# Kernel optimization log

Measured on AMD Instinct MI355X. Metric: run time of the kernel, lower is better.

The kernel has to match this reference:

```python
import jax, jax.numpy as jnp
import numpy as np

# module-level constants from the original repo
NUM_CLASSES = 4
CLASS_NONE = 0
RETINA_SIZE = 224.0

# loss weights (ContourLoss defaults)
POINT_W, ORIENT_W, CLASS_W, INTERSECT_W = 1.0, 0.5, 1.0, 0.1

B, S = 8, 2048


def setup_inputs() -> dict:
    key = jax.random.key(0)
    k1, k2, k3, k4, k5, k6, k7 = jax.random.split(key, 7)
    point_pred = jax.random.uniform(k1, (B, S, 2), jnp.float32) * RETINA_SIZE
    orient_pred = jax.random.normal(k2, (B, S, 2), jnp.float32)
    orient_pred = orient_pred / jnp.linalg.norm(orient_pred, axis=-1, keepdims=True)
    class_pred = jax.random.normal(k3, (B, S, NUM_CLASSES), jnp.float32)
    tgt_pts = jax.random.uniform(k4, (B, S, 2), jnp.float32) * RETINA_SIZE
    tgt_orient = jax.random.normal(k5, (B, S, 2), jnp.float32)
    tgt_orient = tgt_orient / jnp.linalg.norm(tgt_orient, axis=-1, keepdims=True)
    tgt_cls = jax.random.randint(k6, (B, S), 0, NUM_CLASSES).astype(jnp.float32)
    target_seq = jnp.concatenate([tgt_pts, tgt_orient, tgt_cls[..., None]], axis=-1)
    padding_mask = jax.random.bernoulli(k7, 0.15, (B, S))
    return {"point_pred": point_pred, "orient_pred": orient_pred,
            "class_pred": class_pred, "target_seq": target_seq,
            "padding_mask": padding_mask}


def _intersection_per_sample(pts, non_none):
    # pts: (S,2), non_none: (S,) bool.
    # Compact valid points to the front (stable), mirroring point_pred[b, valid_idx].
    order = jnp.argsort(jnp.logical_not(non_none), stable=True)
    pts_c = pts[order]                      # (S,2), first n rows valid
    n = non_none.sum()
    n_seg = n - 1
    starts, ends = pts_c[:-1], pts_c[1:]    # (S-1,2)
    M = S - 1
    ii = jnp.arange(M)[:, None]
    jj = jnp.arange(M)[None, :]
    mask = ((jj >= ii + 2) & (ii < n_seg) & (jj < n_seg)
            & ~((ii == 0) & (jj == n_seg - 1)) & (n >= 4))
    p1 = starts[:, None, :]; p2 = ends[:, None, :]   # segment i
    p3 = starts[None, :, :]; p4 = ends[None, :, :]   # segment j

    def cross(a, b, c):
        return ((b[..., 0] - a[..., 0]) * (c[..., 1] - a[..., 1])
                - (b[..., 1] - a[..., 1]) * (c[..., 0] - a[..., 0]))

    d1 = cross(p3, p4, p1)
    d2 = cross(p3, p4, p2)
    d3 = cross(p1, p2, p3)
    d4 = cross(p1, p2, p4)
    s = jax.nn.sigmoid(-d1 * d2 * 0.01) * jax.nn.sigmoid(-d3 * d4 * 0.01)
    return jnp.where(mask, s, 0.0).sum(), mask.sum()


def reference(point_pred, orient_pred, class_pred, target_seq, padding_mask):
    Bd, Sd, _ = class_pred.shape
    target_class = target_seq[:, :, 4].astype(jnp.int32)
    target_point = target_seq[:, :, :2]
    target_orient = target_seq[:, :, 2:4]
    valid = jnp.logical_not(padding_mask)
    valid_f = valid.astype(jnp.float32)

    # classification: cross entropy, masked mean over valid tokens
    logp = jax.nn.log_softmax(class_pred, axis=-1)
    cls = -jnp.take_along_axis(logp, target_class[..., None], axis=-1)[..., 0]
    cls_loss = (cls * valid_f).sum() / jnp.maximum(valid_f.sum(), 1.0)

    non_none = valid & (target_class != CLASS_NONE)
    nn_f = non_none.astype(jnp.float32)
    nn_denom = jnp.maximum(nn_f.sum(), 1.0)

    # point: SmoothL1 (beta=1) on normalized coords, mean over xy, masked mean
    d = (point_pred - target_point) / RETINA_SIZE
    ad = jnp.abs(d)
    sl1 = jnp.where(ad < 1.0, 0.5 * d * d, ad - 0.5).mean(axis=-1)
    pt_loss = (sl1 * nn_f).sum() / nn_denom

    # orientation: 1 - cosine similarity (orient_pred assumed L2-normalized)
    cos_sim = (orient_pred * target_orient).sum(axis=-1)
    orient_loss = ((1.0 - cos_sim) * nn_f).sum() / nn_denom

    # intersection penalty over non-adjacent segment pairs, per sample
    sums, counts = jax.vmap(_intersection_per_sample)(point_pred, non_none)
    cnt = counts.sum()
    intersect_loss = jnp.where(cnt > 0, sums.sum() / jnp.maximum(cnt, 1).astype(jnp.float32), 0.0)

    total = (POINT_W * pt_loss + ORIENT_W * orient_loss
             + CLASS_W * cls_loss + INTERSECT_W * intersect_loss)
    return (total, pt_loss, orient_loss, cls_loss, intersect_loss)
```

## Files before the change

kernel.cpp:

```cpp
#include <hip/hip_runtime.h>

#define B 8
#define S 2048
#define NBPS 64
#define NBLK (B * NBPS)
#define TPB 256
#define LPB (S / NBPS)


__global__ __launch_bounds__(TPB) void mega_kernel(
    const float2* __restrict__ point_pred,
    const float2* __restrict__ orient_pred,
    const float4* __restrict__ class_pred,
    const float*  __restrict__ target_seq,
    const int*    __restrict__ padding_mask,
    int*   __restrict__ n_buf,
    float* __restrict__ partial,
    float* __restrict__ acc2)
{
    __shared__ float2 sp[S];
    __shared__ float red[TPB / 64][1];
    __shared__ int wsum[TPB / 64], woff[TPB / 64], nTot;

    const int blk = blockIdx.x;
    const int tid = threadIdx.x;
    const int lane = tid & 63, wv = tid >> 6;
    const int b = blk >> 6;
    const int iblk = blk & (NBPS - 1);
    const int base = b * S;
    const int e0 = tid * 8;

    const int4* pm4 = (const int4*)(padding_mask + base + e0);
    const int4 ma = pm4[0], mb = pm4[1];
    const float4* tr4 = (const float4*)(target_seq + (size_t)(base + e0) * 5);
    float4 tq[10];
    #pragma unroll
    for (int k = 0; k < 10; ++k) tq[k] = tr4[k];
    float t4v[8];
    t4v[0] = tq[1].x; t4v[1] = tq[2].y; t4v[2] = tq[3].z; t4v[3] = tq[4].w;
    t4v[4] = tq[6].x; t4v[5] = tq[7].y; t4v[6] = tq[8].z; t4v[7] = tq[9].w;
    const float4* pq4 = (const float4*)(point_pred + base + e0);
    const float4 pa = pq4[0], pb = pq4[1], pc = pq4[2], pd = pq4[3];
    float2 p[8];
    p[0] = make_float2(pa.x, pa.y); p[1] = make_float2(pa.z, pa.w);
    p[2] = make_float2(pb.x, pb.y); p[3] = make_float2(pb.z, pb.w);
    p[4] = make_float2(pc.x, pc.y); p[5] = make_float2(pc.z, pc.w);
    p[6] = make_float2(pd.x, pd.y); p[7] = make_float2(pd.z, pd.w);
    int f[8];
    f[0] = (ma.x == 0 && (int)t4v[0] != 0) ? 1 : 0;
    f[1] = (ma.y == 0 && (int)t4v[1] != 0) ? 1 : 0;
    f[2] = (ma.z == 0 && (int)t4v[2] != 0) ? 1 : 0;
    f[3] = (ma.w == 0 && (int)t4v[3] != 0) ? 1 : 0;
    f[4] = (mb.x == 0 && (int)t4v[4] != 0) ? 1 : 0;
    f[5] = (mb.y == 0 && (int)t4v[5] != 0) ? 1 : 0;
    f[6] = (mb.z == 0 && (int)t4v[6] != 0) ? 1 : 0;
    f[7] = (mb.w == 0 && (int)t4v[7] != 0) ? 1 : 0;

    float cls_a = 0.f, pt_a = 0.f, or_a = 0.f, v_a = 0.f, nn_a = 0.f;
    if (tid < LPB) {
        const int idx = base + iblk * LPB + tid;
        const bool valid = (padding_mask[idx] == 0);
        const float* row = target_seq + (size_t)idx * 5;
        const float t4 = row[4];
        const int tc = (int)t4;
        const bool nn = valid && (tc != 0);
        if (valid) {
            const float4 cl = class_pred[idx];
            const float m = fmaxf(fmaxf(cl.x, cl.y), fmaxf(cl.z, cl.w));
            const float lse = m + logf(expf(cl.x - m) + expf(cl.y - m) +
                                       expf(cl.z - m) + expf(cl.w - m));
            const float ct = (tc == 0) ? cl.x : (tc == 1) ? cl.y : (tc == 2) ? cl.z : cl.w;
            cls_a = lse - ct;
            v_a = 1.f;
        }
        if (nn) {
            const float2 pp = point_pred[idx];
            const float dx = (pp.x - row[0]) * (1.0f / 224.0f);
            const float dy = (pp.y - row[1]) * (1.0f / 224.0f);
            const float adx = fabsf(dx), ady = fabsf(dy);
            const float l0 = (adx < 1.f) ? 0.5f * dx * dx : adx - 0.5f;
            const float l1 = (ady < 1.f) ? 0.5f * dy * dy : ady - 0.5f;
            pt_a = 0.5f * (l0 + l1);
            const float2 op = orient_pred[idx];
            or_a = 1.f - (op.x * row[2] + op.y * row[3]);
            nn_a = 1.f;
        }
    }
    if (wv == 0) {
        #pragma unroll
        for (int off = 32; off > 0; off >>= 1) {
            cls_a += __shfl_down(cls_a, (unsigned)off, 64);
            pt_a  += __shfl_down(pt_a,  (unsigned)off, 64);
            or_a  += __shfl_down(or_a,  (unsigned)off, 64);
            v_a   += __shfl_down(v_a,   (unsigned)off, 64);
            nn_a  += __shfl_down(nn_a,  (unsigned)off, 64);
        }
        if (lane == 0) {
            acc2[0 * NBLK + blk] = cls_a;
            acc2[1 * NBLK + blk] = pt_a;
            acc2[2 * NBLK + blk] = or_a;
            acc2[3 * NBLK + blk] = v_a;
            acc2[4 * NBLK + blk] = nn_a;
        }
    }

    const int c = f[0]+f[1]+f[2]+f[3]+f[4]+f[5]+f[6]+f[7];
    int inc = c;
    #pragma unroll
    for (int off = 1; off < 64; off <<= 1) {
        int u = __shfl_up(inc, (unsigned)off, 64);
        if (lane >= off) inc += u;
    }
    if (lane == 63) wsum[wv] = inc;
    __syncthreads();
    if (tid == 0) {
        int run = 0;
        #pragma unroll
        for (int w = 0; w < TPB / 64; ++w) { woff[w] = run; run += wsum[w]; }
        nTot = run;
    }
    __syncthreads();
    int pos = woff[wv] + inc - c;
    #pragma unroll
    for (int k = 0; k < 8; ++k) { if (f[k]) sp[pos++] = p[k]; }
    __syncthreads();

    const int n = nTot;
    if (iblk == 0 && tid == 0) n_buf[b] = n;

    float local = 0.f;
    if (n >= 4) {
        const int n_seg = n - 1;
        for (int i = iblk; i < n_seg - 2; i += NBPS) {
            const float2 q1 = sp[i], q2 = sp[i + 1];
            const float e12x = q2.x - q1.x, e12y = q2.y - q1.y;
            const int jmax = (i == 0) ? n_seg - 1 : n_seg;
            for (int j = i + 2 + tid; j < jmax; j += TPB) {
                const float2 q3 = sp[j], q4 = sp[j + 1];
                const float e34x = q4.x - q3.x, e34y = q4.y - q3.y;
                const float ce = e12x * e34y - e12y * e34x;
                const float rx = q1.x - q3.x, ry = q1.y - q3.y;
                const float d1 = e34x * ry - e34y * rx;
                const float d3 = e12y * rx - e12x * ry;
                const float d2 = d1 - ce;
                const float d4 = d3 + ce;
                const float ea = __expf(d1 * d2 * 0.01f);
                const float eb = __expf(d3 * d4 * 0.01f);
                local += __builtin_amdgcn_rcpf((1.f + ea) * (1.f + eb));
            }
        }
    }
    #pragma unroll
    for (int off = 32; off > 0; off >>= 1)
        local += __shfl_down(local, (unsigned)off, 64);
    if (lane == 0) red[wv][0] = local;
    __syncthreads();
    if (tid == 0)
        partial[blk] = red[0][0] + red[1][0] + red[2][0] + red[3][0];
}

__global__ __launch_bounds__(64) void finalize_kernel(
    const float* __restrict__ acc2,
    const int* __restrict__ n_buf,
    const float* __restrict__ partial,
    float* __restrict__ out)
{
    const int lane = threadIdx.x;

    const float4* p4 = (const float4*)partial;
    const float4 u = p4[lane * 2], v = p4[lane * 2 + 1];
    float s = (u.x + u.y) + (u.z + u.w) + (v.x + v.y) + (v.z + v.w);

    float a[5];
    #pragma unroll
    for (int ch = 0; ch < 5; ++ch) {
        const float4* c4 = (const float4*)(acc2 + ch * NBLK);
        const float4 x = c4[lane * 2], y = c4[lane * 2 + 1];
        a[ch] = (x.x + x.y) + (x.z + x.w) + (y.x + y.y) + (y.z + y.w);
    }

    #pragma unroll
    for (int off = 32; off > 0; off >>= 1) {
        s += __shfl_down(s, (unsigned)off, 64);
        #pragma unroll
        for (int ch = 0; ch < 5; ++ch)
            a[ch] += __shfl_down(a[ch], (unsigned)off, 64);
    }

    if (lane == 0) {
        const float inter_sum = s;
        long long cnt = 0;
        #pragma unroll
        for (int b2 = 0; b2 < B; ++b2) {
            const int n = n_buf[b2];
            if (n >= 4) {
                const long long ns = n - 1;
                cnt += (ns - 1) * (ns - 2) / 2 - 1;
            }
        }
        const float cls_loss = a[0] / fmaxf(a[3], 1.f);
        const float pt_loss = a[1] / fmaxf(a[4], 1.f);
        const float orient_loss = a[2] / fmaxf(a[4], 1.f);
        const float intersect_loss = (cnt > 0) ? inter_sum / (float)cnt : 0.f;
        out[0] = 1.0f * pt_loss + 0.5f * orient_loss +
                 1.0f * cls_loss + 0.1f * intersect_loss;
        out[1] = pt_loss;
        out[2] = orient_loss;
        out[3] = cls_loss;
        out[4] = intersect_loss;
    }
}

extern "C" void kernel_launch(void* const* d_in, const int* in_sizes, int n_in,
                              void* d_out, int out_size, void* d_ws, size_t ws_size,
                              hipStream_t stream) {
    (void)in_sizes; (void)n_in; (void)out_size; (void)ws_size;
    const float2* point_pred  = (const float2*)d_in[0];
    const float2* orient_pred = (const float2*)d_in[1];
    const float4* class_pred  = (const float4*)d_in[2];
    const float*  target_seq  = (const float*)d_in[3];
    const int*    padding_mask = (const int*)d_in[4];

    int*   n_buf   = (int*)d_ws;
    float* partial = (float*)((char*)d_ws + 64);
    float* acc2    = (float*)((char*)d_ws + 2176);

    mega_kernel<<<NBLK, TPB, 0, stream>>>(point_pred, orient_pred, class_pred,
                                          target_seq, padding_mask,
                                          n_buf, partial, acc2);
    finalize_kernel<<<1, 64, 0, stream>>>(acc2, n_buf, partial, (float*)d_out);
}
```

Baseline: 22.20 us.

## Split loss and intersection work into separate blocks and double intersection blocks per sample

Intersection blocks per sample go from 64 to 128, so each block handles fewer segment rows i, giving 1024 intersection blocks. The per-element loss terms move out of those blocks into 64 dedicated blocks that use all 256 threads, and each block reduces the five accumulators in shared memory before writing them. The finalize kernel is updated for the new partial and accumulator layouts. In exchange, every intersection block still reloads and compacts its whole sample, so that redundant load and scan work now happens twice as often.

```diff
diff --git a/kernel.cpp b/kernel.cpp
--- a/kernel.cpp
+++ b/kernel.cpp
@@ -2,10 +2,11 @@
 
 #define B 8
 #define S 2048
-#define NBPS 64
-#define NBLK (B * NBPS)
+#define NBPS 128
+#define NBLK_INTER (B * NBPS)
+#define NBLK_LOSS 64
+#define NBLK_TOTAL (NBLK_INTER + NBLK_LOSS)
 #define TPB 256
-#define LPB (S / NBPS)
 
 
 __global__ __launch_bounds__(TPB) void mega_kernel(
@@ -19,51 +20,105 @@
     float* __restrict__ acc2)
 {
     __shared__ float2 sp[S];
-    __shared__ float red[TPB / 64][1];
+    __shared__ float red[TPB / 64][5];
     __shared__ int wsum[TPB / 64], woff[TPB / 64], nTot;
 
     const int blk = blockIdx.x;
     const int tid = threadIdx.x;
     const int lane = tid & 63, wv = tid >> 6;
-    const int b = blk >> 6;
-    const int iblk = blk & (NBPS - 1);
-    const int base = b * S;
-    const int e0 = tid * 8;
-
-    const int4* pm4 = (const int4*)(padding_mask + base + e0);
-    const int4 ma = pm4[0], mb = pm4[1];
-    const float4* tr4 = (const float4*)(target_seq + (size_t)(base + e0) * 5);
-    float4 tq[10];
-    #pragma unroll
-    for (int k = 0; k < 10; ++k) tq[k] = tr4[k];
-    float t4v[8];
-    t4v[0] = tq[1].x; t4v[1] = tq[2].y; t4v[2] = tq[3].z; t4v[3] = tq[4].w;
-    t4v[4] = tq[6].x; t4v[5] = tq[7].y; t4v[6] = tq[8].z; t4v[7] = tq[9].w;
-    const float4* pq4 = (const float4*)(point_pred + base + e0);
-    const float4 pa = pq4[0], pb = pq4[1], pc = pq4[2], pd = pq4[3];
-    float2 p[8];
-    p[0] = make_float2(pa.x, pa.y); p[1] = make_float2(pa.z, pa.w);
-    p[2] = make_float2(pb.x, pb.y); p[3] = make_float2(pb.z, pb.w);
-    p[4] = make_float2(pc.x, pc.y); p[5] = make_float2(pc.z, pc.w);
-    p[6] = make_float2(pd.x, pd.y); p[7] = make_float2(pd.z, pd.w);
-    int f[8];
-    f[0] = (ma.x == 0 && (int)t4v[0] != 0) ? 1 : 0;
-    f[1] = (ma.y == 0 && (int)t4v[1] != 0) ? 1 : 0;
-    f[2] = (ma.z == 0 && (int)t4v[2] != 0) ? 1 : 0;
-    f[3] = (ma.w == 0 && (int)t4v[3] != 0) ? 1 : 0;
-    f[4] = (mb.x == 0 && (int)t4v[4] != 0) ? 1 : 0;
-    f[5] = (mb.y == 0 && (int)t4v[5] != 0) ? 1 : 0;
-    f[6] = (mb.z == 0 && (int)t4v[6] != 0) ? 1 : 0;
-    f[7] = (mb.w == 0 && (int)t4v[7] != 0) ? 1 : 0;
-
-    float cls_a = 0.f, pt_a = 0.f, or_a = 0.f, v_a = 0.f, nn_a = 0.f;
-    if (tid < LPB) {
-        const int idx = base + iblk * LPB + tid;
+
+    if (blk < NBLK_INTER) {
+        const int b = blk >> 7;
+        const int iblk = blk & (NBPS - 1);
+        const int base = b * S;
+        const int e0 = tid * 8;
+
+        const int4* pm4 = (const int4*)(padding_mask + base + e0);
+        const int4 ma = pm4[0], mb = pm4[1];
+        const float4* tr4 = (const float4*)(target_seq + (size_t)(base + e0) * 5);
+        float4 tq[10];
+        #pragma unroll
+        for (int k = 0; k < 10; ++k) tq[k] = tr4[k];
+        float t4v[8];
+        t4v[0] = tq[1].x; t4v[1] = tq[2].y; t4v[2] = tq[3].z; t4v[3] = tq[4].w;
+        t4v[4] = tq[6].x; t4v[5] = tq[7].y; t4v[6] = tq[8].z; t4v[7] = tq[9].w;
+        const float4* pq4 = (const float4*)(point_pred + base + e0);
+        const float4 pa = pq4[0], pb = pq4[1], pc = pq4[2], pd = pq4[3];
+        float2 p[8];
+        p[0] = make_float2(pa.x, pa.y); p[1] = make_float2(pa.z, pa.w);
+        p[2] = make_float2(pb.x, pb.y); p[3] = make_float2(pb.z, pb.w);
+        p[4] = make_float2(pc.x, pc.y); p[5] = make_float2(pc.z, pc.w);
+        p[6] = make_float2(pd.x, pd.y); p[7] = make_float2(pd.z, pd.w);
+        int f[8];
+        f[0] = (ma.x == 0 && (int)t4v[0] != 0) ? 1 : 0;
+        f[1] = (ma.y == 0 && (int)t4v[1] != 0) ? 1 : 0;
+        f[2] = (ma.z == 0 && (int)t4v[2] != 0) ? 1 : 0;
+        f[3] = (ma.w == 0 && (int)t4v[3] != 0) ? 1 : 0;
+        f[4] = (mb.x == 0 && (int)t4v[4] != 0) ? 1 : 0;
+        f[5] = (mb.y == 0 && (int)t4v[5] != 0) ? 1 : 0;
+        f[6] = (mb.z == 0 && (int)t4v[6] != 0) ? 1 : 0;
+        f[7] = (mb.w == 0 && (int)t4v[7] != 0) ? 1 : 0;
+
+        const int c = f[0]+f[1]+f[2]+f[3]+f[4]+f[5]+f[6]+f[7];
+        int inc = c;
+        #pragma unroll
+        for (int off = 1; off < 64; off <<= 1) {
+            int u = __shfl_up(inc, (unsigned)off, 64);
+            if (lane >= off) inc += u;
+        }
+        if (lane == 63) wsum[wv] = inc;
+        __syncthreads();
+        if (tid == 0) {
+            int run = 0;
+            #pragma unroll
+            for (int w = 0; w < TPB / 64; ++w) { woff[w] = run; run += wsum[w]; }
+            nTot = run;
+        }
+        __syncthreads();
+        int pos = woff[wv] + inc - c;
+        #pragma unroll
+        for (int k = 0; k < 8; ++k) { if (f[k]) sp[pos++] = p[k]; }
+        __syncthreads();
+
+        const int n = nTot;
+        if (iblk == 0 && tid == 0) n_buf[b] = n;
+
+        float local = 0.f;
+        if (n >= 4) {
+            const int n_seg = n - 1;
+            for (int i = iblk; i < n_seg - 2; i += NBPS) {
+                const float2 q1 = sp[i], q2 = sp[i + 1];
+                const float e12x = q2.x - q1.x, e12y = q2.y - q1.y;
+                const int jmax = (i == 0) ? n_seg - 1 : n_seg;
+                for (int j = i + 2 + tid; j < jmax; j += TPB) {
+                    const float2 q3 = sp[j], q4 = sp[j + 1];
+                    const float e34x = q4.x - q3.x, e34y = q4.y - q3.y;
+                    const float ce = e12x * e34y - e12y * e34x;
+                    const float rx = q1.x - q3.x, ry = q1.y - q3.y;
+                    const float d1 = e34x * ry - e34y * rx;
+                    const float d3 = e12y * rx - e12x * ry;
+                    const float d2 = d1 - ce;
+                    const float d4 = d3 + ce;
+                    const float ea = __expf(d1 * d2 * 0.01f);
+                    const float eb = __expf(d3 * d4 * 0.01f);
+                    local += __builtin_amdgcn_rcpf((1.f + ea) * (1.f + eb));
+                }
+            }
+        }
+        #pragma unroll
+        for (int off = 32; off > 0; off >>= 1)
+            local += __shfl_down(local, (unsigned)off, 64);
+        if (lane == 0) red[wv][0] = local;
+        __syncthreads();
+        if (tid == 0)
+            partial[blk] = red[0][0] + red[1][0] + red[2][0] + red[3][0];
+    } else {
+        const int idx = (blk - NBLK_INTER) * TPB + tid;
         const bool valid = (padding_mask[idx] == 0);
-        const float* row = target_seq + (size_t)idx * 5;
-        const float t4 = row[4];
+        const float t4 = target_seq[(size_t)idx * 5 + 4];
         const int tc = (int)t4;
         const bool nn = valid && (tc != 0);
+        float cls_a = 0.f, pt_a = 0.f, or_a = 0.f, v_a = 0.f, nn_a = 0.f;
         if (valid) {
             const float4 cl = class_pred[idx];
             const float m = fmaxf(fmaxf(cl.x, cl.y), fmaxf(cl.z, cl.w));
@@ -75,18 +130,20 @@
         }
         if (nn) {
             const float2 pp = point_pred[idx];
-            const float dx = (pp.x - row[0]) * (1.0f / 224.0f);
-            const float dy = (pp.y - row[1]) * (1.0f / 224.0f);
+            const float tx = target_seq[(size_t)idx * 5 + 0];
+            const float ty = target_seq[(size_t)idx * 5 + 1];
+            const float dx = (pp.x - tx) * (1.0f / 224.0f);
+            const float dy = (pp.y - ty) * (1.0f / 224.0f);
             const float adx = fabsf(dx), ady = fabsf(dy);
             const float l0 = (adx < 1.f) ? 0.5f * dx * dx : adx - 0.5f;
             const float l1 = (ady < 1.f) ? 0.5f * dy * dy : ady - 0.5f;
             pt_a = 0.5f * (l0 + l1);
             const float2 op = orient_pred[idx];
-            or_a = 1.f - (op.x * row[2] + op.y * row[3]);
+            const float ox = target_seq[(size_t)idx * 5 + 2];
+            const float oy = target_seq[(size_t)idx * 5 + 3];
+            or_a = 1.f - (op.x * ox + op.y * oy);
             nn_a = 1.f;
         }
-    }
-    if (wv == 0) {
         #pragma unroll
         for (int off = 32; off > 0; off >>= 1) {
             cls_a += __shfl_down(cls_a, (unsigned)off, 64);
@@ -96,67 +153,18 @@
             nn_a  += __shfl_down(nn_a,  (unsigned)off, 64);
         }
         if (lane == 0) {
-            acc2[0 * NBLK + blk] = cls_a;
-            acc2[1 * NBLK + blk] = pt_a;
-            acc2[2 * NBLK + blk] = or_a;
-            acc2[3 * NBLK + blk] = v_a;
-            acc2[4 * NBLK + blk] = nn_a;
-        }
-    }
-
-    const int c = f[0]+f[1]+f[2]+f[3]+f[4]+f[5]+f[6]+f[7];
-    int inc = c;
-    #pragma unroll
-    for (int off = 1; off < 64; off <<= 1) {
-        int u = __shfl_up(inc, (unsigned)off, 64);
-        if (lane >= off) inc += u;
-    }
-    if (lane == 63) wsum[wv] = inc;
-    __syncthreads();
-    if (tid == 0) {
-        int run = 0;
-        #pragma unroll
-        for (int w = 0; w < TPB / 64; ++w) { woff[w] = run; run += wsum[w]; }
-        nTot = run;
-    }
-    __syncthreads();
-    int pos = woff[wv] + inc - c;
-    #pragma unroll
-    for (int k = 0; k < 8; ++k) { if (f[k]) sp[pos++] = p[k]; }
-    __syncthreads();
-
-    const int n = nTot;
-    if (iblk == 0 && tid == 0) n_buf[b] = n;
-
-    float local = 0.f;
-    if (n >= 4) {
-        const int n_seg = n - 1;
-        for (int i = iblk; i < n_seg - 2; i += NBPS) {
-            const float2 q1 = sp[i], q2 = sp[i + 1];
-            const float e12x = q2.x - q1.x, e12y = q2.y - q1.y;
-            const int jmax = (i == 0) ? n_seg - 1 : n_seg;
-            for (int j = i + 2 + tid; j < jmax; j += TPB) {
-                const float2 q3 = sp[j], q4 = sp[j + 1];
-                const float e34x = q4.x - q3.x, e34y = q4.y - q3.y;
-                const float ce = e12x * e34y - e12y * e34x;
-                const float rx = q1.x - q3.x, ry = q1.y - q3.y;
-                const float d1 = e34x * ry - e34y * rx;
-                const float d3 = e12y * rx - e12x * ry;
-                const float d2 = d1 - ce;
-                const float d4 = d3 + ce;
-                const float ea = __expf(d1 * d2 * 0.01f);
-                const float eb = __expf(d3 * d4 * 0.01f);
-                local += __builtin_amdgcn_rcpf((1.f + ea) * (1.f + eb));
-            }
-        }
-    }
-    #pragma unroll
-    for (int off = 32; off > 0; off >>= 1)
-        local += __shfl_down(local, (unsigned)off, 64);
-    if (lane == 0) red[wv][0] = local;
-    __syncthreads();
-    if (tid == 0)
-        partial[blk] = red[0][0] + red[1][0] + red[2][0] + red[3][0];
+            red[wv][0] = cls_a; red[wv][1] = pt_a; red[wv][2] = or_a;
+            red[wv][3] = v_a;   red[wv][4] = nn_a;
+        }
+        __syncthreads();
+        if (tid == 0) {
+            const int lb = blk - NBLK_INTER;
+            #pragma unroll
+            for (int c5 = 0; c5 < 5; ++c5)
+                acc2[c5 * NBLK_LOSS + lb] =
+                    red[0][c5] + red[1][c5] + red[2][c5] + red[3][c5];
+        }
+    }
 }
 
 __global__ __launch_bounds__(64) void finalize_kernel(
@@ -168,16 +176,16 @@
     const int lane = threadIdx.x;
 
     const float4* p4 = (const float4*)partial;
-    const float4 u = p4[lane * 2], v = p4[lane * 2 + 1];
-    float s = (u.x + u.y) + (u.z + u.w) + (v.x + v.y) + (v.z + v.w);
+    float s = 0.f;
+    #pragma unroll
+    for (int k = 0; k < 4; ++k) {
+        const float4 u = p4[lane * 4 + k];
+        s += (u.x + u.y) + (u.z + u.w);
+    }
 
     float a[5];
     #pragma unroll
-    for (int ch = 0; ch < 5; ++ch) {
-        const float4* c4 = (const float4*)(acc2 + ch * NBLK);
-        const float4 x = c4[lane * 2], y = c4[lane * 2 + 1];
-        a[ch] = (x.x + x.y) + (x.z + x.w) + (y.x + y.y) + (y.z + y.w);
-    }
+    for (int ch = 0; ch < 5; ++ch) a[ch] = acc2[ch * NBLK_LOSS + lane];
 
     #pragma unroll
     for (int off = 32; off > 0; off >>= 1) {
@@ -223,10 +231,11 @@
 
     int*   n_buf   = (int*)d_ws;
     float* partial = (float*)((char*)d_ws + 64);
-    float* acc2    = (float*)((char*)d_ws + 2176);
-
-    mega_kernel<<<NBLK, TPB, 0, stream>>>(point_pred, orient_pred, class_pred,
-                                          target_seq, padding_mask,
-                                          n_buf, partial, acc2);
+    float* acc2    = (float*)((char*)d_ws + 4224);
+
+    mega_kernel<<<NBLK_TOTAL, TPB, 0, stream>>>(point_pred, orient_pred,
+                                                class_pred, target_seq,
+                                                padding_mask,
+                                                n_buf, partial, acc2);
     finalize_kernel<<<1, 64, 0, stream>>>(acc2, n_buf, partial, (float*)d_out);
 }
```

Result: faster. 19.76 us (-11.0%).
